# Performance work log

Hardware: AMD Instinct MI355X
Metric: run time of the kernel (lower is better)

## Reference

```python
import jax, jax.numpy as jnp
import numpy as np

BATCH = 32768
Z_IN = 24
X_DIM = (2, 32, 16)
X_FLAT = X_DIM[0] * X_DIM[1] * X_DIM[2]  # 1024
EPS = 1e-5


def _bn(x, g, b):
    # BatchNorm1d with track_running_stats=False: always batch stats, biased var
    m = x.mean(0)
    v = x.var(0)
    return g * (x - m) / jnp.sqrt(v + EPS) + b


def _linear_params(k, fan_in, fan_out):
    lim = 1.0 / np.sqrt(fan_in)
    kw, kb = jax.random.split(k)
    W = jax.random.uniform(kw, (fan_in, fan_out), minval=-lim, maxval=lim, dtype=jnp.float32)
    b = jax.random.uniform(kb, (fan_out,), minval=-lim, maxval=lim, dtype=jnp.float32)
    return W, b


def setup_inputs() -> dict:
    key = jax.random.key(0)
    ks = jax.random.split(key, 6)
    z = jax.random.normal(ks[0], (BATCH, Z_IN), dtype=jnp.float32)
    W1, b1 = _linear_params(ks[1], Z_IN, 300)
    W2, b2 = _linear_params(ks[2], 300, 400)
    W3, b3 = _linear_params(ks[3], 400, X_FLAT)
    Wa1, ba1 = _linear_params(ks[4], 300, 150)
    Wa2, ba2 = _linear_params(ks[5], 150, 63)
    return {
        "z": z,
        "W1": W1, "b1": b1, "g1": jnp.ones(300, jnp.float32), "be1": jnp.zeros(300, jnp.float32),
        "W2": W2, "b2": b2, "g2": jnp.ones(400, jnp.float32), "be2": jnp.zeros(400, jnp.float32),
        "W3": W3, "b3": b3,
        "Wa1": Wa1, "ba1": ba1, "ga": jnp.ones(150, jnp.float32), "bea": jnp.zeros(150, jnp.float32),
        "Wa2": Wa2, "ba2": ba2,
    }


def _forward(z, W1, b1, g1, be1, W2, b2, g2, be2, W3, b3, Wa1, ba1, ga, bea, Wa2, ba2):
    B = z.shape[0]
    h = _bn(jax.nn.relu(z.reshape(B, -1) @ W1 + b1), g1, be1)          # (B,300)
    m = _bn(jax.nn.relu(h @ W2 + b2), g2, be2)                         # (B,400)
    mu_out = (m @ W3 + b3).reshape(B, *X_DIM)                          # (B,2,32,16)

    a = _bn(jax.nn.relu(h @ Wa1 + ba1), ga, bea) @ Wa2 + ba2           # (B,63)
    a0 = jnp.minimum(jnp.exp(a[:, 0]), 500.0)[:, None, None]          # (B,1,1)
    ar = 0.022 * a0 * jnp.tanh(a[:, None, 1:])                         # (B,1,62)
    ar_c = (ar[:, :, :31] + 1j * ar[:, :, 31:]).astype(jnp.complex64)  # (B,1,31)
    Alpha = jnp.concatenate([a0.astype(jnp.complex64), ar_c], axis=2)  # (B,1,32)
    Alpha_p = jnp.concatenate(
        [jnp.zeros((B, 1, 1), jnp.complex64), Alpha[:, :, :0:-1]], axis=2)  # (B,1,32)

    # Toeplitz gather: values has length 63, torch negative indexing == wrap mod 63
    off = jnp.arange(32)[None, :] - jnp.arange(32)[:, None]            # j - i
    idx = off % 63                                                     # (32,32)
    B_mask = jnp.tril(jnp.ones((32, 32), jnp.float32))[None, None]
    C_mask = jnp.tril(jnp.ones((32, 32), jnp.float32), -1)[None, None]

    values = jnp.concatenate([Alpha, Alpha[:, :, :0:-1]], axis=2)      # (B,1,63)
    Bmat = values[:, :, idx] * B_mask                                  # (B,1,32,32) complex

    values_p = jnp.concatenate([Alpha_p, Alpha_p[:, :, :0:-1]], axis=2)
    Cmat = jnp.conj(values_p[:, :, idx] * C_mask)                      # (B,1,32,32) complex
    return mu_out, Bmat, Cmat


def reference(z, W1, b1, g1, be1, W2, b2, g2, be2, W3, b3, Wa1, ba1, ga, bea, Wa2, ba2):
    return _forward(z, W1, b1, g1, be1, W2, b2, g2, be2, W3, b3, Wa1, ba1, ga, bea, Wa2, ba2)
```

## Files before the change

### kernel.cpp

```cpp
#include <hip/hip_runtime.h>
#include <hip/hip_bf16.h>


#define BATCH_N 32768
#define EPSF 1e-5f

typedef __attribute__((ext_vector_type(4))) float f32x4;
typedef __attribute__((ext_vector_type(8))) short bf16x8;
typedef unsigned short ushort_t;

__device__ inline void bf16split(float v, unsigned short& h, unsigned short& l) {
  unsigned u = __float_as_uint(v);
  h = (unsigned short)(u >> 16);
  float hf = __uint_as_float((unsigned)h << 16);
  float r = v - hf;
  l = (unsigned short)(__float_as_uint(r) >> 16);
}

#define TM 128
#define TN 128
#define TKK 16

__global__ __launch_bounds__(256) void gemm_l1(
    const float* __restrict__ A, const float* __restrict__ W,
    const float* __restrict__ bias,
    ushort_t* __restrict__ Ch, ushort_t* __restrict__ Cl, int Kpo,
    float* __restrict__ gsum, float* __restrict__ gsq,
    int M, int N, int K) {
  __shared__ float As[TKK][TM + 4];
  __shared__ float Ws[TKK][TN];
  __shared__ float lsum[TN], lsq[TN];
  const int tid = threadIdx.x;
  const int tx = tid & 15;
  const int ty = tid >> 4;
  const int m0 = blockIdx.y * TM;
  const int n0 = blockIdx.x * TN;

  if (tid < TN) { lsum[tid] = 0.f; lsq[tid] = 0.f; }

  float acc[8][8];
#pragma unroll
  for (int i = 0; i < 8; ++i)
#pragma unroll
    for (int j = 0; j < 8; ++j) acc[i][j] = 0.f;

  for (int k0 = 0; k0 < K; k0 += TKK) {
#pragma unroll
    for (int l = 0; l < 8; ++l) {
      int idx = tid + l * 256;
      int m = idx >> 4, k = idx & 15;
      As[k][m] = (k0 + k < K) ? A[(size_t)(m0 + m) * K + (k0 + k)] : 0.f;
    }
#pragma unroll
    for (int l = 0; l < 8; ++l) {
      int idx = tid + l * 256;
      int k = idx >> 7, n = idx & 127;
      float v = 0.f;
      if ((k0 + k < K) && (n0 + n < N)) v = W[(size_t)(k0 + k) * N + (n0 + n)];
      Ws[k][n] = v;
    }
    __syncthreads();
#pragma unroll
    for (int kk = 0; kk < TKK; ++kk) {
      float a[8], w[8];
      *(float4*)&a[0] = *(const float4*)&As[kk][ty * 8];
      *(float4*)&a[4] = *(const float4*)&As[kk][ty * 8 + 4];
      *(float4*)&w[0] = *(const float4*)&Ws[kk][tx * 4];
      *(float4*)&w[4] = *(const float4*)&Ws[kk][64 + tx * 4];
#pragma unroll
      for (int i = 0; i < 8; ++i)
#pragma unroll
        for (int j = 0; j < 8; ++j) acc[i][j] = fmaf(a[i], w[j], acc[i][j]);
    }
    __syncthreads();
  }

#pragma unroll
  for (int j = 0; j < 8; ++j) {
    const int lc = (j < 4) ? (tx * 4 + j) : (64 + tx * 4 + (j - 4));
    const int col = n0 + lc;
    if (col >= N) continue;
    const float bv = bias[col];
    float ps = 0.f, pq = 0.f;
#pragma unroll
    for (int i = 0; i < 8; ++i) {
      const int row = m0 + ty * 8 + i;
      float v = fmaxf(acc[i][j] + bv, 0.f);
      ps += v; pq += v * v;
      unsigned short h, l;
      bf16split(v, h, l);
      Ch[(size_t)row * Kpo + col] = h;
      Cl[(size_t)row * Kpo + col] = l;
    }
    atomicAdd(&lsum[lc], ps);
    atomicAdd(&lsq[lc], pq);
  }
  __syncthreads();
  if (tid < TN && n0 + tid < N) {
    atomicAdd(&gsum[n0 + tid], lsum[tid]);
    atomicAdd(&gsq[n0 + tid], lsq[tid]);
  }
}

#define GTM 128
#define GTN 128
#define GBK 32
#define LPAD 40

template <bool RELU, bool STATS, bool SPLITOUT>
__global__ __launch_bounds__(256) void gemm_mfma2(
    const ushort_t* __restrict__ Ah, const ushort_t* __restrict__ Al,
    const ushort_t* __restrict__ Wth, const ushort_t* __restrict__ Wtl,
    const float* __restrict__ bias,
    float* __restrict__ Cf, int ldc,
    ushort_t* __restrict__ Ch, ushort_t* __restrict__ Cl, int Kpo,
    float* __restrict__ gsum, float* __restrict__ gsq,
    int M, int N, int K, int Kp) {
  __shared__ ushort_t Ahs[GTM * LPAD];
  __shared__ ushort_t Als[GTM * LPAD];
  __shared__ ushort_t Whs[GTN * LPAD];
  __shared__ ushort_t Wls[GTN * LPAD];

  const int tid = threadIdx.x;
  const int lane = tid & 63;
  const int wave = tid >> 6;
  const int wr = wave >> 1;
  const int wc = wave & 1;
  const int m0 = blockIdx.y * GTM;
  const int n0 = blockIdx.x * GTN;

  const int sm = tid >> 1;
  const int sk = (tid & 1) * 16;

  f32x4 acc[4][4];
#pragma unroll
  for (int mi = 0; mi < 4; ++mi)
#pragma unroll
    for (int ni = 0; ni < 4; ++ni)
#pragma unroll
      for (int q = 0; q < 4; ++q) acc[mi][ni][q] = 0.f;

  const int lrow = lane & 15;
  const int lko = (lane >> 4) * 8;

  for (int k0 = 0; k0 < K; k0 += GBK) {
    {
      const size_t aoff = (size_t)(m0 + sm) * Kp + k0 + sk;
      *(bf16x8*)&Ahs[sm * LPAD + sk]     = *(const bf16x8*)(Ah + aoff);
      *(bf16x8*)&Ahs[sm * LPAD + sk + 8] = *(const bf16x8*)(Ah + aoff + 8);
      *(bf16x8*)&Als[sm * LPAD + sk]     = *(const bf16x8*)(Al + aoff);
      *(bf16x8*)&Als[sm * LPAD + sk + 8] = *(const bf16x8*)(Al + aoff + 8);
    }
    {
      const int ng = n0 + sm;
      bf16x8 h0 = {0,0,0,0,0,0,0,0}, h1 = h0, l0 = h0, l1 = h0;
      if (ng < N) {
        const size_t off = (size_t)ng * Kp + k0 + sk;
        h0 = *(const bf16x8*)(Wth + off);
        h1 = *(const bf16x8*)(Wth + off + 8);
        l0 = *(const bf16x8*)(Wtl + off);
        l1 = *(const bf16x8*)(Wtl + off + 8);
      }
      *(bf16x8*)&Whs[sm * LPAD + sk]     = h0;
      *(bf16x8*)&Whs[sm * LPAD + sk + 8] = h1;
      *(bf16x8*)&Wls[sm * LPAD + sk]     = l0;
      *(bf16x8*)&Wls[sm * LPAD + sk + 8] = l1;
    }
    __syncthreads();

    bf16x8 afh[4], afl[4];
#pragma unroll
    for (int mi = 0; mi < 4; ++mi) {
      const int r = wr * 64 + mi * 16 + lrow;
      afh[mi] = *(const bf16x8*)&Ahs[r * LPAD + lko];
      afl[mi] = *(const bf16x8*)&Als[r * LPAD + lko];
    }
#pragma unroll
    for (int ni = 0; ni < 4; ++ni) {
      const int c = wc * 64 + ni * 16 + lrow;
      bf16x8 bh = *(const bf16x8*)&Whs[c * LPAD + lko];
      bf16x8 bl = *(const bf16x8*)&Wls[c * LPAD + lko];
#pragma unroll
      for (int mi = 0; mi < 4; ++mi) {
        acc[mi][ni] = __builtin_amdgcn_mfma_f32_16x16x32_bf16(afh[mi], bh, acc[mi][ni], 0, 0, 0);
        acc[mi][ni] = __builtin_amdgcn_mfma_f32_16x16x32_bf16(afl[mi], bh, acc[mi][ni], 0, 0, 0);
        acc[mi][ni] = __builtin_amdgcn_mfma_f32_16x16x32_bf16(afh[mi], bl, acc[mi][ni], 0, 0, 0);
      }
    }
    __syncthreads();
  }

  float ps[4], pq[4];
#pragma unroll
  for (int ni = 0; ni < 4; ++ni) { ps[ni] = 0.f; pq[ni] = 0.f; }

#pragma unroll
  for (int ni = 0; ni < 4; ++ni) {
    const int col = n0 + wc * 64 + ni * 16 + lrow;
    const bool cok = (col < N);
    const float bv = cok ? bias[col] : 0.f;
#pragma unroll
    for (int mi = 0; mi < 4; ++mi) {
      const int rbase = m0 + wr * 64 + mi * 16 + (lane >> 4) * 4;
#pragma unroll
      for (int q = 0; q < 4; ++q) {
        float v = acc[mi][ni][q] + bv;
        if (RELU) v = fmaxf(v, 0.f);
        if (STATS) { ps[ni] += v; pq[ni] += v * v; }
        if (cok) {
          if (SPLITOUT) {
            unsigned short h, l;
            bf16split(v, h, l);
            Ch[(size_t)(rbase + q) * Kpo + col] = h;
            Cl[(size_t)(rbase + q) * Kpo + col] = l;
          } else {
            Cf[(size_t)(rbase + q) * ldc + col] = v;
          }
        }
      }
    }
  }
  if (STATS) {
#pragma unroll
    for (int ni = 0; ni < 4; ++ni) {
      float s = ps[ni], q = pq[ni];
      s += __shfl_xor(s, 16); s += __shfl_xor(s, 32);
      q += __shfl_xor(q, 16); q += __shfl_xor(q, 32);
      const int col = n0 + wc * 64 + ni * 16 + lrow;
      if (lane < 16 && col < N) {
        atomicAdd(&gsum[col], s);
        atomicAdd(&gsq[col], q);
      }
    }
  }
}

__global__ void fold_wt_split(const float* __restrict__ W, const float* __restrict__ s,
                              ushort_t* __restrict__ hi, ushort_t* __restrict__ lo,
                              int K, int N, int Kp) {
  int idx = blockIdx.x * 256 + threadIdx.x;
  if (idx >= N * Kp) return;
  int n = idx / Kp, k = idx - n * Kp;
  float v = 0.f;
  if (k < K) v = W[(size_t)k * N + n] * s[k];
  unsigned short h, l;
  bf16split(v, h, l);
  hi[idx] = h;
  lo[idx] = l;
}

__global__ void fold_bias(const float* __restrict__ W, const float* __restrict__ t,
                          const float* __restrict__ bin, float* __restrict__ bout,
                          int K, int N) {
  int n = blockIdx.x * 256 + threadIdx.x;
  if (n >= N) return;
  float acc = bin[n];
  for (int k = 0; k < K; ++k) acc = fmaf(t[k], W[(size_t)k * N + n], acc);
  bout[n] = acc;
}

__global__ void zero_buf(float* __restrict__ p, int n) {
  int i = blockIdx.x * 256 + threadIdx.x;
  if (i < n) p[i] = 0.f;
}

__global__ void prep_st(const float* __restrict__ sum, const float* __restrict__ sq,
                        const float* __restrict__ g, const float* __restrict__ be,
                        float* __restrict__ s, float* __restrict__ t,
                        int N, float invM) {
  int n = blockIdx.x * 256 + threadIdx.x;
  if (n < N) {
    float mean = sum[n] * invM;
    float var = sq[n] * invM - mean * mean;
    float inv = 1.0f / sqrtf(var + EPSF);
    float sv = g[n] * inv;
    s[n] = sv;
    t[n] = be[n] - mean * sv;
  }
}

#define AROWS 8
__global__ __launch_bounds__(256) void a_toeplitz_real(
    const float* __restrict__ Ra, const float* __restrict__ Wa2,
    const float* __restrict__ ba2, const float* __restrict__ sa,
    const float* __restrict__ ta, float* __restrict__ outB,
    float* __restrict__ outC) {
  __shared__ float Wlh[150 * 32];
  __shared__ float Rl[AROWS][152];
  __shared__ float al[AROWS][33];
  __shared__ float Are[AROWS][33];
  const int tid = threadIdx.x;
  const int b0 = blockIdx.x * AROWS;

  for (int idx = tid; idx < 150 * 32; idx += 256) {
    int k = idx >> 5, j = idx & 31;
    Wlh[idx] = Wa2[k * 63 + j];
  }
  for (int i = tid; i < AROWS * 150; i += 256) {
    int r = i / 150, k = i - r * 150;
    Rl[r][k] = fmaf(sa[k], Ra[(size_t)(b0 + r) * 150 + k], ta[k]);
  }
  __syncthreads();

  {
    const int r = tid >> 5, j = tid & 31;
    float acc = ba2[j];
    for (int k = 0; k < 150; ++k) acc = fmaf(Rl[r][k], Wlh[k * 32 + j], acc);
    al[r][j] = acc;
  }
  __syncthreads();

  {
    const int r = tid >> 5, kk = tid & 31;
    float a0 = fminf(expf(al[r][0]), 500.f);
    Are[r][kk] = (kk == 0) ? a0 : 0.022f * a0 * tanhf(al[r][kk]);
  }
  __syncthreads();

  const int i = tid >> 3;
  const int j0 = (tid & 7) * 4;
  const int d0 = i - j0;
  for (int r = 0; r < AROWS; ++r) {
    const size_t base = (size_t)(b0 + r) * 1024;
    float4 vb, vc;
    vb.x = (d0     >= 0) ? Are[r][d0]     : 0.f;
    vb.y = (d0 - 1 >= 0) ? Are[r][d0 - 1] : 0.f;
    vb.z = (d0 - 2 >= 0) ? Are[r][d0 - 2] : 0.f;
    vb.w = (d0 - 3 >= 0) ? Are[r][d0 - 3] : 0.f;
    vc.x = (d0     >= 1) ? Are[r][32 - d0]       : 0.f;
    vc.y = (d0 - 1 >= 1) ? Are[r][32 - (d0 - 1)] : 0.f;
    vc.z = (d0 - 2 >= 1) ? Are[r][32 - (d0 - 2)] : 0.f;
    vc.w = (d0 - 3 >= 1) ? Are[r][32 - (d0 - 3)] : 0.f;
    *(float4*)(outB + base + (size_t)tid * 4) = vb;
    *(float4*)(outC + base + (size_t)tid * 4) = vc;
  }
}

extern "C" void kernel_launch(void* const* d_in, const int* in_sizes, int n_in,
                              void* d_out, int out_size, void* d_ws, size_t ws_size,
                              hipStream_t stream) {
  const float* z   = (const float*)d_in[0];
  const float* W1  = (const float*)d_in[1];
  const float* b1  = (const float*)d_in[2];
  const float* g1  = (const float*)d_in[3];
  const float* be1 = (const float*)d_in[4];
  const float* W2  = (const float*)d_in[5];
  const float* b2  = (const float*)d_in[6];
  const float* g2  = (const float*)d_in[7];
  const float* be2 = (const float*)d_in[8];
  const float* W3  = (const float*)d_in[9];
  const float* b3  = (const float*)d_in[10];
  const float* Wa1 = (const float*)d_in[11];
  const float* ba1 = (const float*)d_in[12];
  const float* ga  = (const float*)d_in[13];
  const float* bea = (const float*)d_in[14];
  const float* Wa2 = (const float*)d_in[15];
  const float* ba2 = (const float*)d_in[16];

  float* out = (float*)d_out;
  const int B = BATCH_N;
  (void)out_size;

  float* mu   = out;
  float* outB = out + (size_t)B * 1024;
  float* outC = out + (size_t)B * 2048;

  const size_t bytes_needed =
      (size_t)B * 320 * 2 * 2 + (size_t)B * 416 * 2 * 2 +
      (size_t)B * 150 * 4 + 3500 * 4;
  if (ws_size < bytes_needed) return;

  char* wsb = (char*)d_ws;
  ushort_t* R1h = (ushort_t*)wsb;                     wsb += (size_t)B * 320 * 2;
  ushort_t* R1l = (ushort_t*)wsb;                     wsb += (size_t)B * 320 * 2;
  ushort_t* R2h = (ushort_t*)wsb;                     wsb += (size_t)B * 416 * 2;
  ushort_t* R2l = (ushort_t*)wsb;                     wsb += (size_t)B * 416 * 2;
  float* Ra  = (float*)wsb;                           wsb += (size_t)B * 150 * 4;
  float* scr = (float*)wsb;
  float* stats = scr;
  float* sum1 = stats;       float* sq1 = sum1 + 300;
  float* sum2 = sq1 + 300;   float* sq2 = sum2 + 400;
  float* suma = sq2 + 400;   float* sqa = suma + 150;
  float* s1 = scr + 1700;    float* t1 = s1 + 300;
  float* s2 = t1 + 300;      float* t2 = s2 + 400;
  float* sa = t2 + 400;      float* ta = sa + 150;

  ushort_t* us = (ushort_t*)outB;
  ushort_t* WtMu_h = us;
  ushort_t* WtMu_l = WtMu_h + 1024 * 416;
  ushort_t* Wt2_h  = WtMu_l + 1024 * 416;
  ushort_t* Wt2_l  = Wt2_h + 400 * 320;
  ushort_t* Wta_h  = Wt2_l + 400 * 320;
  ushort_t* Wta_l  = Wta_h + 150 * 320;
  float* fb   = (float*)(Wta_l + 150 * 320);
  float* b2f  = fb;
  float* ba1f = fb + 400;
  float* b3f  = fb + 550;

  const dim3 blk(256);
  const float invB = 1.0f / (float)B;

  zero_buf<<<7, blk, 0, stream>>>(stats, 1700);

  gemm_l1<<<dim3(3, B / TM), blk, 0, stream>>>(
      z, W1, b1, R1h, R1l, 320, sum1, sq1, B, 300, 24);
  prep_st<<<2, blk, 0, stream>>>(sum1, sq1, g1, be1, s1, t1, 300, invB);

  fold_wt_split<<<(400 * 320 + 255) / 256, blk, 0, stream>>>(W2, s1, Wt2_h, Wt2_l, 300, 400, 320);
  fold_bias<<<2, blk, 0, stream>>>(W2, t1, b2, b2f, 300, 400);
  fold_wt_split<<<(150 * 320 + 255) / 256, blk, 0, stream>>>(Wa1, s1, Wta_h, Wta_l, 300, 150, 320);
  fold_bias<<<1, blk, 0, stream>>>(Wa1, t1, ba1, ba1f, 300, 150);

  gemm_mfma2<true, true, true><<<dim3(4, B / GTM), blk, 0, stream>>>(
      R1h, R1l, Wt2_h, Wt2_l, b2f, nullptr, 0, R2h, R2l, 416,
      sum2, sq2, B, 400, 300, 320);
  gemm_mfma2<true, true, false><<<dim3(2, B / GTM), blk, 0, stream>>>(
      R1h, R1l, Wta_h, Wta_l, ba1f, Ra, 150, nullptr, nullptr, 0,
      suma, sqa, B, 150, 300, 320);

  prep_st<<<2, blk, 0, stream>>>(sum2, sq2, g2, be2, s2, t2, 400, invB);
  prep_st<<<1, blk, 0, stream>>>(suma, sqa, ga, bea, sa, ta, 150, invB);

  fold_wt_split<<<(1024 * 416 + 255) / 256, blk, 0, stream>>>(W3, s2, WtMu_h, WtMu_l, 400, 1024, 416);
  fold_bias<<<4, blk, 0, stream>>>(W3, t2, b3, b3f, 400, 1024);

  gemm_mfma2<false, false, false><<<dim3(8, B / GTM), blk, 0, stream>>>(
      R2h, R2l, WtMu_h, WtMu_l, b3f, mu, 1024, nullptr, nullptr, 0,
      nullptr, nullptr, B, 1024, 400, 416);

  a_toeplitz_real<<<B / AROWS, blk, 0, stream>>>(
      Ra, Wa2, ba2, sa, ta, outB, outC);
}
```

Baseline: 861.9 us.

## Drop low-bf16 activation terms for mu GEMMs and remap blocks across XCDs

The layer-2 and layer-3 GEMMs now drop the A-low split term. The L2 output is written as a single round-to-nearest bf16 array instead of a hi/lo pair, and the L3 GEMM and L2's read of R1 skip the low activation loads and MFMAs. Padding columns are explicitly zero-filled so the K padding stays clean. The block index is also remapped so consecutive M tiles land on the same XCD for L2 cache locality. This cuts about a third of the MFMA work and much of the activation traffic, at the cost of precision in the mu and layer-2 outputs.

Measured after the change: 766.6 us. 1.12x faster.

```diff
diff --git a/kernel.cpp b/kernel.cpp
--- a/kernel.cpp
+++ b/kernel.cpp
@@ -15,6 +15,11 @@
   float hf = __uint_as_float((unsigned)h << 16);
   float r = v - hf;
   l = (unsigned short)(__float_as_uint(r) >> 16);
+}
+
+__device__ inline unsigned short bf16rne(float v) {
+  unsigned u = __float_as_uint(v);
+  return (unsigned short)((u + 0x7FFFu + ((u >> 16) & 1u)) >> 16);
 }
 
 #define TM 128
@@ -79,21 +84,24 @@
   for (int j = 0; j < 8; ++j) {
     const int lc = (j < 4) ? (tx * 4 + j) : (64 + tx * 4 + (j - 4));
     const int col = n0 + lc;
-    if (col >= N) continue;
-    const float bv = bias[col];
+    if (col >= Kpo) continue;
+    const bool live = (col < N);
+    const float bv = live ? bias[col] : 0.f;
     float ps = 0.f, pq = 0.f;
 #pragma unroll
     for (int i = 0; i < 8; ++i) {
       const int row = m0 + ty * 8 + i;
-      float v = fmaxf(acc[i][j] + bv, 0.f);
+      float v = live ? fmaxf(acc[i][j] + bv, 0.f) : 0.f;
       ps += v; pq += v * v;
       unsigned short h, l;
       bf16split(v, h, l);
       Ch[(size_t)row * Kpo + col] = h;
       Cl[(size_t)row * Kpo + col] = l;
     }
-    atomicAdd(&lsum[lc], ps);
-    atomicAdd(&lsq[lc], pq);
+    if (live) {
+      atomicAdd(&lsum[lc], ps);
+      atomicAdd(&lsq[lc], pq);
+    }
   }
   __syncthreads();
   if (tid < TN && n0 + tid < N) {
@@ -107,17 +115,17 @@
 #define GBK 32
 #define LPAD 40
 
-template <bool RELU, bool STATS, bool SPLITOUT>
-__global__ __launch_bounds__(256) void gemm_mfma2(
+template <bool RELU, bool STATS, bool ALO, bool BF16OUT>
+__global__ __launch_bounds__(256) void gemm_mfma3(
     const ushort_t* __restrict__ Ah, const ushort_t* __restrict__ Al,
     const ushort_t* __restrict__ Wth, const ushort_t* __restrict__ Wtl,
     const float* __restrict__ bias,
     float* __restrict__ Cf, int ldc,
-    ushort_t* __restrict__ Ch, ushort_t* __restrict__ Cl, int Kpo,
+    ushort_t* __restrict__ Cbh, int Kpo,
     float* __restrict__ gsum, float* __restrict__ gsq,
     int M, int N, int K, int Kp) {
   __shared__ ushort_t Ahs[GTM * LPAD];
-  __shared__ ushort_t Als[GTM * LPAD];
+  __shared__ ushort_t Als[ALO ? GTM * LPAD : 64];
   __shared__ ushort_t Whs[GTN * LPAD];
   __shared__ ushort_t Wls[GTN * LPAD];
 
@@ -126,8 +134,15 @@
   const int wave = tid >> 6;
   const int wr = wave >> 1;
   const int wc = wave & 1;
-  const int m0 = blockIdx.y * GTM;
-  const int n0 = blockIdx.x * GTN;
+
+  const int NBx = gridDim.x;
+  const int bflat = blockIdx.y * NBx + blockIdx.x;
+  const int xcd = bflat & 7;
+  const int j = bflat >> 3;
+  const int nb = j % NBx;
+  const int mj = j / NBx;
+  const int m0 = (mj * 8 + xcd) * GTM;
+  const int n0 = nb * GTN;
 
   const int sm = tid >> 1;
   const int sk = (tid & 1) * 16;
@@ -148,8 +163,10 @@
       const size_t aoff = (size_t)(m0 + sm) * Kp + k0 + sk;
       *(bf16x8*)&Ahs[sm * LPAD + sk]     = *(const bf16x8*)(Ah + aoff);
       *(bf16x8*)&Ahs[sm * LPAD + sk + 8] = *(const bf16x8*)(Ah + aoff + 8);
-      *(bf16x8*)&Als[sm * LPAD + sk]     = *(const bf16x8*)(Al + aoff);
-      *(bf16x8*)&Als[sm * LPAD + sk + 8] = *(const bf16x8*)(Al + aoff + 8);
+      if (ALO) {
+        *(bf16x8*)&Als[sm * LPAD + sk]     = *(const bf16x8*)(Al + aoff);
+        *(bf16x8*)&Als[sm * LPAD + sk + 8] = *(const bf16x8*)(Al + aoff + 8);
+      }
     }
     {
       const int ng = n0 + sm;
@@ -173,7 +190,7 @@
     for (int mi = 0; mi < 4; ++mi) {
       const int r = wr * 64 + mi * 16 + lrow;
       afh[mi] = *(const bf16x8*)&Ahs[r * LPAD + lko];
-      afl[mi] = *(const bf16x8*)&Als[r * LPAD + lko];
+      if (ALO) afl[mi] = *(const bf16x8*)&Als[r * LPAD + lko];
     }
 #pragma unroll
     for (int ni = 0; ni < 4; ++ni) {
@@ -183,8 +200,9 @@
 #pragma unroll
       for (int mi = 0; mi < 4; ++mi) {
         acc[mi][ni] = __builtin_amdgcn_mfma_f32_16x16x32_bf16(afh[mi], bh, acc[mi][ni], 0, 0, 0);
-        acc[mi][ni] = __builtin_amdgcn_mfma_f32_16x16x32_bf16(afl[mi], bh, acc[mi][ni], 0, 0, 0);
         acc[mi][ni] = __builtin_amdgcn_mfma_f32_16x16x32_bf16(afh[mi], bl, acc[mi][ni], 0, 0, 0);
+        if (ALO)
+          acc[mi][ni] = __builtin_amdgcn_mfma_f32_16x16x32_bf16(afl[mi], bh, acc[mi][ni], 0, 0, 0);
       }
     }
     __syncthreads();
@@ -197,25 +215,20 @@
 #pragma unroll
   for (int ni = 0; ni < 4; ++ni) {
     const int col = n0 + wc * 64 + ni * 16 + lrow;
-    const bool cok = (col < N);
-    const float bv = cok ? bias[col] : 0.f;
+    const bool live = (col < N);
+    const float bv = live ? bias[col] : 0.f;
 #pragma unroll
     for (int mi = 0; mi < 4; ++mi) {
       const int rbase = m0 + wr * 64 + mi * 16 + (lane >> 4) * 4;
 #pragma unroll
       for (int q = 0; q < 4; ++q) {
-        float v = acc[mi][ni][q] + bv;
+        float v = live ? (acc[mi][ni][q] + bv) : 0.f;
         if (RELU) v = fmaxf(v, 0.f);
         if (STATS) { ps[ni] += v; pq[ni] += v * v; }
-        if (cok) {
-          if (SPLITOUT) {
-            unsigned short h, l;
-            bf16split(v, h, l);
-            Ch[(size_t)(rbase + q) * Kpo + col] = h;
-            Cl[(size_t)(rbase + q) * Kpo + col] = l;
-          } else {
-            Cf[(size_t)(rbase + q) * ldc + col] = v;
-          }
+        if (BF16OUT) {
+          if (col < Kpo) Cbh[(size_t)(rbase + q) * Kpo + col] = live ? bf16rne(v) : 0;
+        } else {
+          if (live) Cf[(size_t)(rbase + q) * ldc + col] = v;
         }
       }
     }
@@ -366,16 +379,15 @@
   float* outC = out + (size_t)B * 2048;
 
   const size_t bytes_needed =
-      (size_t)B * 320 * 2 * 2 + (size_t)B * 416 * 2 * 2 +
+      (size_t)B * 320 * 2 * 2 + (size_t)B * 416 * 2 +
       (size_t)B * 150 * 4 + 3500 * 4;
   if (ws_size < bytes_needed) return;
 
   char* wsb = (char*)d_ws;
-  ushort_t* R1h = (ushort_t*)wsb;                     wsb += (size_t)B * 320 * 2;
-  ushort_t* R1l = (ushort_t*)wsb;                     wsb += (size_t)B * 320 * 2;
-  ushort_t* R2h = (ushort_t*)wsb;                     wsb += (size_t)B * 416 * 2;
-  ushort_t* R2l = (ushort_t*)wsb;                     wsb += (size_t)B * 416 * 2;
-  float* Ra  = (float*)wsb;                           wsb += (size_t)B * 150 * 4;
+  ushort_t* R1h = (ushort_t*)wsb;                wsb += (size_t)B * 320 * 2;
+  ushort_t* R1l = (ushort_t*)wsb;                wsb += (size_t)B * 320 * 2;
+  ushort_t* R2h = (ushort_t*)wsb;                wsb += (size_t)B * 416 * 2;
+  float* Ra  = (float*)wsb;                      wsb += (size_t)B * 150 * 4;
   float* scr = (float*)wsb;
   float* stats = scr;
   float* sum1 = stats;       float* sq1 = sum1 + 300;
@@ -411,11 +423,11 @@
   fold_wt_split<<<(150 * 320 + 255) / 256, blk, 0, stream>>>(Wa1, s1, Wta_h, Wta_l, 300, 150, 320);
   fold_bias<<<1, blk, 0, stream>>>(Wa1, t1, ba1, ba1f, 300, 150);
 
-  gemm_mfma2<true, true, true><<<dim3(4, B / GTM), blk, 0, stream>>>(
-      R1h, R1l, Wt2_h, Wt2_l, b2f, nullptr, 0, R2h, R2l, 416,
+  gemm_mfma3<true, true, false, true><<<dim3(4, B / GTM), blk, 0, stream>>>(
+      R1h, nullptr, Wt2_h, Wt2_l, b2f, nullptr, 0, R2h, 416,
       sum2, sq2, B, 400, 300, 320);
-  gemm_mfma2<true, true, false><<<dim3(2, B / GTM), blk, 0, stream>>>(
-      R1h, R1l, Wta_h, Wta_l, ba1f, Ra, 150, nullptr, nullptr, 0,
+  gemm_mfma3<true, true, true, false><<<dim3(2, B / GTM), blk, 0, stream>>>(
+      R1h, R1l, Wta_h, Wta_l, ba1f, Ra, 150, nullptr, 0,
       suma, sqa, B, 150, 300, 320);
 
   prep_st<<<2, blk, 0, stream>>>(sum2, sq2, g2, be2, s2, t2, 400, invB);
@@ -424,8 +436,8 @@
   fold_wt_split<<<(1024 * 416 + 255) / 256, blk, 0, stream>>>(W3, s2, WtMu_h, WtMu_l, 400, 1024, 416);
   fold_bias<<<4, blk, 0, stream>>>(W3, t2, b3, b3f, 400, 1024);
 
-  gemm_mfma2<false, false, false><<<dim3(8, B / GTM), blk, 0, stream>>>(
-      R2h, R2l, WtMu_h, WtMu_l, b3f, mu, 1024, nullptr, nullptr, 0,
+  gemm_mfma3<false, false, false, false><<<dim3(8, B / GTM), blk, 0, stream>>>(
+      R2h, nullptr, WtMu_h, WtMu_l, b3f, mu, 1024, nullptr, 0,
       nullptr, nullptr, B, 1024, 400, 416);
 
   a_toeplitz_real<<<B / AROWS, blk, 0, stream>>>(
```
